# Kernel tuning notes

Measured on AMD Instinct MI355X. Metric: run time of the kernel, lower is better.

Reference implementation:

```python
import jax, jax.numpy as jnp
import numpy as np

TEMPERATURE = 0.5


def setup_inputs() -> dict:
    key = jax.random.key(0)
    k1, k2 = jax.random.split(key)
    N, D = 4096, 512
    emb_i = jax.random.normal(k1, (N, D), dtype=jnp.float32)
    emb_j = jax.random.normal(k2, (N, D), dtype=jnp.float32)
    return {"emb_i": emb_i, "emb_j": emb_j}


def reference(emb_i, emb_j):
    # L2-normalize each embedding row (F.normalize, dim=1)
    z_i = emb_i / jnp.linalg.norm(emb_i, axis=1, keepdims=True)
    z_j = emb_j / jnp.linalg.norm(emb_j, axis=1, keepdims=True)
    reps = jnp.concatenate([z_i, z_j], axis=0)  # [2N, D]
    N = emb_i.shape[0]
    M = 2 * N
    # cosine similarity of normalized vectors == dot product -> [2N, 2N]
    sim = jnp.einsum('id,jd->ij', reps, reps) / TEMPERATURE
    # denominator: sum_k!=i exp(sim[i,k]); original multiplies by one-hot complement
    exp_sim = jnp.exp(sim)
    denom = jnp.sum(exp_sim, axis=1) - jnp.diagonal(exp_sim)  # [2N]
    log_denom = jnp.log(denom)
    # positive pairs: (k, k+N) and (k+N, k)
    idx = jnp.arange(N)
    pos_ij = sim[idx, idx + N]          # sim(k, k+N)/T
    pos_ji = sim[idx + N, idx]          # sim(k+N, k)/T
    loss = jnp.sum(-(pos_ij - log_denom[:N]) - (pos_ji - log_denom[N:]))
    return loss / (2.0 * N)
```

## Files before the change

kernel.cpp:

```cpp
#include <hip/hip_runtime.h>
#include <cstdint>
#include <cstddef>

constexpr int N_ROWS = 4096;
constexpr int D      = 512;
constexpr int M      = 8192;
constexpr int NTILE  = 64;
constexpr int NBLK   = NTILE * (NTILE + 1) / 2;
constexpr int BKB    = 64;
constexpr int LDSB   = 128 * BKB;

using f32x4 = __attribute__((ext_vector_type(4))) float;
using ul2   = __attribute__((ext_vector_type(2))) unsigned long;

#define ASYNC_CP16(gsrc, ldst)                                                      \
    __builtin_amdgcn_global_load_lds(                                               \
        (const __attribute__((address_space(1))) unsigned int*)(gsrc),              \
        (__attribute__((address_space(3))) unsigned int*)(ldst), 16, 0, 0)

#define SS_FP8(pk, accum)                                                           \
    do {                                                                            \
        float f0 = __builtin_amdgcn_cvt_f32_fp8((pk), 0);                           \
        float f1 = __builtin_amdgcn_cvt_f32_fp8((pk), 1);                           \
        float f2 = __builtin_amdgcn_cvt_f32_fp8((pk), 2);                           \
        float f3 = __builtin_amdgcn_cvt_f32_fp8((pk), 3);                           \
        (accum) += f0 * f0 + f1 * f1 + f2 * f2 + f3 * f3;                           \
    } while (0)

__global__ __launch_bounds__(256) void normpos_kernel(
    const float* __restrict__ emb_i, const float* __restrict__ emb_j,
    uint8_t* __restrict__ zb, float* __restrict__ diagss,
    float* __restrict__ pos)
{
    const int wave = threadIdx.x >> 6, lane = threadIdx.x & 63;
    const int k = blockIdx.x * 4 + wave;

    const float4* a = (const float4*)(emb_i + (size_t)k * D);
    const float4* b = (const float4*)(emb_j + (size_t)k * D);
    float4 a0 = a[lane * 2], a1 = a[lane * 2 + 1];
    float4 b0 = b[lane * 2], b1 = b[lane * 2 + 1];

    float ssi = a0.x*a0.x + a0.y*a0.y + a0.z*a0.z + a0.w*a0.w
              + a1.x*a1.x + a1.y*a1.y + a1.z*a1.z + a1.w*a1.w;
    float ssj = b0.x*b0.x + b0.y*b0.y + b0.z*b0.z + b0.w*b0.w
              + b1.x*b1.x + b1.y*b1.y + b1.z*b1.z + b1.w*b1.w;
    float dp  = a0.x*b0.x + a0.y*b0.y + a0.z*b0.z + a0.w*b0.w
              + a1.x*b1.x + a1.y*b1.y + a1.z*b1.z + a1.w*b1.w;
    #pragma unroll
    for (int off = 32; off; off >>= 1) {
        ssi += __shfl_xor(ssi, off, 64);
        ssj += __shfl_xor(ssj, off, 64);
        dp  += __shfl_xor(dp,  off, 64);
    }
    const float invi = rsqrtf(ssi), invj = rsqrtf(ssj);

    const float zi[8] = {a0.x*invi, a0.y*invi, a0.z*invi, a0.w*invi,
                         a1.x*invi, a1.y*invi, a1.z*invi, a1.w*invi};
    const float zj[8] = {b0.x*invj, b0.y*invj, b0.z*invj, b0.w*invj,
                         b1.x*invj, b1.y*invj, b1.z*invj, b1.w*invj};

    int pi0 = __builtin_amdgcn_cvt_pk_fp8_f32(zi[0], zi[1], 0, false);
    pi0     = __builtin_amdgcn_cvt_pk_fp8_f32(zi[2], zi[3], pi0, true);
    int pi1 = __builtin_amdgcn_cvt_pk_fp8_f32(zi[4], zi[5], 0, false);
    pi1     = __builtin_amdgcn_cvt_pk_fp8_f32(zi[6], zi[7], pi1, true);
    int pj0 = __builtin_amdgcn_cvt_pk_fp8_f32(zj[0], zj[1], 0, false);
    pj0     = __builtin_amdgcn_cvt_pk_fp8_f32(zj[2], zj[3], pj0, true);
    int pj1 = __builtin_amdgcn_cvt_pk_fp8_f32(zj[4], zj[5], 0, false);
    pj1     = __builtin_amdgcn_cvt_pk_fp8_f32(zj[6], zj[7], pj1, true);

    float dssi = 0.f, dssj = 0.f;
    SS_FP8(pi0, dssi);
    SS_FP8(pi1, dssi);
    SS_FP8(pj0, dssj);
    SS_FP8(pj1, dssj);

    const int g = lane, bb = g >> 3, w = g & 7;
    const int sl = bb * 8 + ((w < 4) ? (w * 2) : ((w - 4) * 2 + 1));
    const unsigned long long vi =
        ((unsigned long long)(unsigned)pi1 << 32) | (unsigned)pi0;
    const unsigned long long vj =
        ((unsigned long long)(unsigned)pj1 << 32) | (unsigned)pj0;
    *(unsigned long long*)(zb + (size_t)k * D + sl * 8)            = vi;
    *(unsigned long long*)(zb + (size_t)(k + N_ROWS) * D + sl * 8) = vj;

    #pragma unroll
    for (int off = 32; off; off >>= 1) {
        dssi += __shfl_xor(dssi, off, 64);
        dssj += __shfl_xor(dssj, off, 64);
    }
    if (lane == 0) {
        diagss[k]          = dssi;
        diagss[k + N_ROWS] = dssj;
        pos[k]             = 2.0f * dp * invi * invj;
    }
}

__global__ __launch_bounds__(256, 4) void simgemm_kernel(
    const uint8_t* __restrict__ zb, float* __restrict__ partials)
{
    __shared__ ul2 AsV[2 * LDSB / 16];
    __shared__ ul2 BsV[2 * LDSB / 16];
    __shared__ float rp[4][64];
    __shared__ float cp4[4][64];
    uint8_t* As = (uint8_t*)AsV;
    uint8_t* Bs = (uint8_t*)BsV;

    const int tid  = threadIdx.x;
    const int wave = tid >> 6, lane = tid & 63;
    const int l15  = lane & 15, ks = lane >> 4;

    const int t = blockIdx.x;
    int bi = (int)((129.0f - sqrtf(129.0f * 129.0f - 8.0f * (float)t)) * 0.5f);
    while (bi > 0 && bi * (129 - bi) / 2 > t) --bi;
    while ((bi + 1) * (129 - (bi + 1)) / 2 <= t) ++bi;
    const int bj = bi + (t - bi * (129 - bi) / 2);
    const bool diag = (bi == bj);

    const int wrow = (wave >> 1) * 64, wcol = (wave & 1) * 64;

    const int srow = wave * 32 + (lane >> 2);
    const int scol = ((lane & 3) ^ ((lane >> 3) & 3)) * 16;
    const uint8_t* gA = zb + (size_t)(bi * 128 + srow) * D + scol;
    const uint8_t* gB = zb + (size_t)(bj * 128 + srow) * D + scol;
    uint8_t* lA = As + wave * 32 * BKB;
    uint8_t* lB = Bs + wave * 32 * BKB;

    ASYNC_CP16(gA,            lA);
    ASYNC_CP16(gA + 16 * D,   lA + 16 * BKB);
    ASYNC_CP16(gB,            lB);
    ASYNC_CP16(gB + 16 * D,   lB + 16 * BKB);

    f32x4 acc[4][4] = {};
    const int swb = (ks ^ ((l15 >> 1) & 3)) * 16;

    for (int it = 0; it < D / BKB; ++it) {
        __syncthreads();

        if (it + 1 < D / BKB) {
            const int kc  = (it + 1) * BKB;
            const int off = ((it + 1) & 1) * LDSB;
            ASYNC_CP16(gA + kc,          lA + off);
            ASYNC_CP16(gA + kc + 16 * D, lA + off + 16 * BKB);
            ASYNC_CP16(gB + kc,          lB + off);
            ASYNC_CP16(gB + kc + 16 * D, lB + off + 16 * BKB);
        }

        const int cb = (it & 1) * LDSB;
        ul2 af[4], bg[4];
        #pragma unroll
        for (int f = 0; f < 4; ++f) {
            af[f] = *(const ul2*)(As + cb + (wrow + f * 16 + l15) * BKB + swb);
            bg[f] = *(const ul2*)(Bs + cb + (wcol + f * 16 + l15) * BKB + swb);
        }
        #pragma unroll
        for (int i = 0; i < 4; ++i)
            #pragma unroll
            for (int j = 0; j < 4; ++j) {
                acc[i][j] = __builtin_amdgcn_mfma_f32_16x16x32_fp8_fp8(
                    (long)af[i][0], (long)bg[j][0], acc[i][j], 0, 0, 0);
                acc[i][j] = __builtin_amdgcn_mfma_f32_16x16x32_fp8_fp8(
                    (long)af[i][1], (long)bg[j][1], acc[i][j], 0, 0, 0);
            }
    }

    float rowp[4][4] = {};
    #pragma unroll
    for (int j = 0; j < 4; ++j) {
        float cpj = 0.f;
        #pragma unroll
        for (int i = 0; i < 4; ++i)
            #pragma unroll
            for (int r = 0; r < 4; ++r) {
                float e = __expf(2.0f * acc[i][j][r]);
                rowp[i][r] += e;
                cpj += e;
            }
        if (!diag) {
            cpj += __shfl_xor(cpj, 16, 64);
            cpj += __shfl_xor(cpj, 32, 64);
            if (ks == 0) cp4[wave][j * 16 + l15] = cpj;
        }
    }
    #pragma unroll
    for (int i = 0; i < 4; ++i)
        #pragma unroll
        for (int r = 0; r < 4; ++r) {
            float e = rowp[i][r];
            e += __shfl_xor(e, 1, 64);
            e += __shfl_xor(e, 2, 64);
            e += __shfl_xor(e, 4, 64);
            e += __shfl_xor(e, 8, 64);
            if (l15 == 0) rp[wave][i * 16 + ks * 4 + r] = e;
        }
    __syncthreads();

    float* pA = partials + (size_t)(bi * NTILE + bj) * 128;
    float* pB = partials + (size_t)(bj * NTILE + bi) * 128;
    if (tid < 128) {
        const int h = tid >> 6, rr = tid & 63;
        pA[tid] = rp[h * 2][rr] + rp[h * 2 + 1][rr];
    } else if (!diag) {
        const int c = tid - 128, h = c >> 6, cc = c & 63;
        pB[c] = cp4[h][cc] + cp4[h + 2][cc];
    }
}

__global__ __launch_bounds__(256) void rowfin_kernel(
    const float* __restrict__ partials, const float* __restrict__ diagss,
    const float* __restrict__ pos, float* __restrict__ lgpart)
{
    const int r  = blockIdx.x;
    const int ri = threadIdx.x & 127;
    const int ch = threadIdx.x >> 7;
    const float* base = partials + (size_t)r * NTILE * 128 + ri;
    float s = 0.f;
    #pragma unroll
    for (int c = 0; c < 32; ++c)
        s += base[(size_t)(ch * 32 + c) * 128];
    __shared__ float half1[128];
    __shared__ float red[4];
    if (ch == 1) half1[ri] = s;
    __syncthreads();
    float lg = 0.f;
    if (ch == 0) {
        float rs = s + half1[ri];
        int row = r * 128 + ri;
        lg = __logf(rs - __expf(2.0f * diagss[row]));
    }
    if (threadIdx.x < 64)
        lg -= 2.0f * pos[r * 64 + threadIdx.x];
    #pragma unroll
    for (int off = 32; off; off >>= 1) lg += __shfl_xor(lg, off, 64);
    const int wave = threadIdx.x >> 6, lane = threadIdx.x & 63;
    if (lane == 0) red[wave] = lg;
    __syncthreads();
    if (threadIdx.x == 0) lgpart[r] = red[0] + red[1] + red[2] + red[3];
}

__global__ __launch_bounds__(64) void loss_kernel(
    const float* __restrict__ lgpart, float* __restrict__ out)
{
    float local = lgpart[threadIdx.x];
    #pragma unroll
    for (int off = 32; off; off >>= 1) local += __shfl_xor(local, off, 64);
    if (threadIdx.x == 0) out[0] = local * (1.0f / 8192.0f);
}

extern "C" void kernel_launch(void* const* d_in, const int* in_sizes, int n_in,
                              void* d_out, int out_size, void* d_ws, size_t ws_size,
                              hipStream_t stream)
{
    const float* emb_i = (const float*)d_in[0];
    const float* emb_j = (const float*)d_in[1];

    uint8_t* zb = (uint8_t*)d_ws;
    float* partials = (float*)((char*)d_ws + (size_t)M * D);
    float* diagss   = partials + (size_t)NTILE * NTILE * 128;
    float* pos      = diagss + M;
    float* lgpart   = pos + N_ROWS;
    float* out      = (float*)d_out;

    normpos_kernel<<<N_ROWS / 4, 256, 0, stream>>>(emb_i, emb_j, zb, diagss, pos);
    simgemm_kernel<<<NBLK, 256, 0, stream>>>(zb, partials);
    rowfin_kernel<<<NTILE, 256, 0, stream>>>(partials, diagss, pos, lgpart);
    loss_kernel<<<1, 64, 0, stream>>>(lgpart, out);
}
```

Measured before the change: 103.4 us.

## Use 256x128 tiles with 512 threads and triple-buffered async LDS pipeline

Changes the symmetric similarity GEMM from 128x128 upper-triangular tiles with 256 threads to 256x128 jobs with 8 waves, where the A panel is shared by two row strips. It also replaces double buffering with a three-stage async global-to-LDS pipeline with explicit vmcnt/lgkmcnt waits, split MFMA phases and setprio hints. The aim is more operand reuse per load, fewer blocks and better overlap of memory with MFMA. The cost is a larger LDS footprint, which may lower occupancy, and a more intricate job indexing where diagonal jobs compute some redundant tiles.

```diff
diff --git a/kernel.cpp b/kernel.cpp
--- a/kernel.cpp
+++ b/kernel.cpp
@@ -6,9 +6,12 @@
 constexpr int D      = 512;
 constexpr int M      = 8192;
 constexpr int NTILE  = 64;
-constexpr int NBLK   = NTILE * (NTILE + 1) / 2;
+constexpr int NJOB   = 1056;
 constexpr int BKB    = 64;
-constexpr int LDSB   = 128 * BKB;
+constexpr int NKT    = D / BKB;
+constexpr int ATB    = 256 * BKB;
+constexpr int BTB    = 128 * BKB;
+constexpr int TILEB  = ATB + BTB;
 
 using f32x4 = __attribute__((ext_vector_type(4))) float;
 using ul2   = __attribute__((ext_vector_type(2))) unsigned long;
@@ -95,113 +98,146 @@
     }
 }
 
-__global__ __launch_bounds__(256, 4) void simgemm_kernel(
+#define MM2(AC, AF, BF)                                                             \
+    do {                                                                            \
+        AC = __builtin_amdgcn_mfma_f32_16x16x32_fp8_fp8(                            \
+                 (long)(AF)[0], (long)(BF)[0], AC, 0, 0, 0);                        \
+        AC = __builtin_amdgcn_mfma_f32_16x16x32_fp8_fp8(                            \
+                 (long)(AF)[1], (long)(BF)[1], AC, 0, 0, 0);                        \
+    } while (0)
+
+__global__ __launch_bounds__(512, 4) void simgemm_kernel(
     const uint8_t* __restrict__ zb, float* __restrict__ partials)
 {
-    __shared__ ul2 AsV[2 * LDSB / 16];
-    __shared__ ul2 BsV[2 * LDSB / 16];
-    __shared__ float rp[4][64];
-    __shared__ float cp4[4][64];
-    uint8_t* As = (uint8_t*)AsV;
-    uint8_t* Bs = (uint8_t*)BsV;
+    __shared__ ul2 ldsV[3 * TILEB / 16];
+    __shared__ float rp[8][64];
+    __shared__ float cp[8][64];
+    uint8_t* lds = (uint8_t*)ldsV;
 
     const int tid  = threadIdx.x;
     const int wave = tid >> 6, lane = tid & 63;
     const int l15  = lane & 15, ks = lane >> 4;
 
     const int t = blockIdx.x;
-    int bi = (int)((129.0f - sqrtf(129.0f * 129.0f - 8.0f * (float)t)) * 0.5f);
-    while (bi > 0 && bi * (129 - bi) / 2 > t) --bi;
-    while ((bi + 1) * (129 - (bi + 1)) / 2 <= t) ++bi;
-    const int bj = bi + (t - bi * (129 - bi) / 2);
-    const bool diag = (bi == bj);
-
-    const int wrow = (wave >> 1) * 64, wcol = (wave & 1) * 64;
-
-    const int srow = wave * 32 + (lane >> 2);
-    const int scol = ((lane & 3) ^ ((lane >> 3) & 3)) * 16;
-    const uint8_t* gA = zb + (size_t)(bi * 128 + srow) * D + scol;
-    const uint8_t* gB = zb + (size_t)(bj * 128 + srow) * D + scol;
-    uint8_t* lA = As + wave * 32 * BKB;
-    uint8_t* lB = Bs + wave * 32 * BKB;
-
-    ASYNC_CP16(gA,            lA);
-    ASYNC_CP16(gA + 16 * D,   lA + 16 * BKB);
-    ASYNC_CP16(gB,            lB);
-    ASYNC_CP16(gB + 16 * D,   lB + 16 * BKB);
+    int i = (int)((65.0f - sqrtf(4225.0f - 4.0f * (float)t)) * 0.5f);
+    if (i < 0) i = 0;
+    if (i > 31) i = 31;
+    while (i > 0 && i * (65 - i) > t) --i;
+    while ((i + 1) * (65 - (i + 1)) <= t) ++i;
+    const int j = 2 * i + (t - i * (65 - i));
+    const bool diagcls = (j - 2 * i) < 2;
+
+    const int srow = tid >> 2;
+    const int sch  = (tid & 3) ^ ((srow >> 1) & 3);
+    const uint8_t* gA = zb + (size_t)(i * 256 + srow) * D + sch * 16;
+    const uint8_t* gB = zb + (size_t)(j * 128 + srow) * D + sch * 16;
+    uint8_t* lw = lds + wave * 1024;
+
+#define STAGE(KT, BUF)                                                              \
+    do {                                                                            \
+        const uint8_t* _a = gA + (KT) * BKB;                                        \
+        const uint8_t* _b = gB + (KT) * BKB;                                        \
+        uint8_t* _l = lw + (BUF) * TILEB;                                           \
+        ASYNC_CP16(_a,           _l);                                               \
+        ASYNC_CP16(_a + 128 * D, _l + 8192);                                        \
+        ASYNC_CP16(_b,           _l + ATB);                                         \
+    } while (0)
+
+    const int wr  = wave >> 1, wc = wave & 1;
+    const int swb = (ks ^ ((l15 >> 1) & 3)) * 16;
+    const int aof = (wr * 64 + l15) * BKB + swb;
+    const int bof = ATB + (wc * 64 + l15) * BKB + swb;
 
     f32x4 acc[4][4] = {};
-    const int swb = (ks ^ ((l15 >> 1) & 3)) * 16;
-
-    for (int it = 0; it < D / BKB; ++it) {
-        __syncthreads();
-
-        if (it + 1 < D / BKB) {
-            const int kc  = (it + 1) * BKB;
-            const int off = ((it + 1) & 1) * LDSB;
-            ASYNC_CP16(gA + kc,          lA + off);
-            ASYNC_CP16(gA + kc + 16 * D, lA + off + 16 * BKB);
-            ASYNC_CP16(gB + kc,          lB + off);
-            ASYNC_CP16(gB + kc + 16 * D, lB + off + 16 * BKB);
+
+    STAGE(0, 0);
+    STAGE(1, 1);
+    asm volatile("s_waitcnt vmcnt(3)" ::: "memory");
+    __builtin_amdgcn_s_barrier();
+
+    #pragma unroll
+    for (int kt = 0; kt < NKT; ++kt) {
+        const uint8_t* La = lds + (kt % 3) * TILEB;
+
+        ul2 a0 = *(const ul2*)(La + aof);
+        ul2 a1 = *(const ul2*)(La + aof + 1024);
+        ul2 b0 = *(const ul2*)(La + bof);
+        ul2 b1 = *(const ul2*)(La + bof + 1024);
+        ul2 b2 = *(const ul2*)(La + bof + 2048);
+        ul2 b3 = *(const ul2*)(La + bof + 3072);
+        if (kt + 2 < NKT) STAGE(kt + 2, (kt + 2) % 3);
+        __builtin_amdgcn_s_barrier();
+        asm volatile("s_waitcnt lgkmcnt(0)" ::: "memory");
+        __builtin_amdgcn_sched_barrier(0);
+        __builtin_amdgcn_s_setprio(1);
+        MM2(acc[0][0], a0, b0); MM2(acc[0][1], a0, b1);
+        MM2(acc[0][2], a0, b2); MM2(acc[0][3], a0, b3);
+        MM2(acc[1][0], a1, b0); MM2(acc[1][1], a1, b1);
+        MM2(acc[1][2], a1, b2); MM2(acc[1][3], a1, b3);
+        __builtin_amdgcn_s_setprio(0);
+        __builtin_amdgcn_s_barrier();
+
+        ul2 a2 = *(const ul2*)(La + aof + 2048);
+        ul2 a3 = *(const ul2*)(La + aof + 3072);
+        __builtin_amdgcn_s_barrier();
+        asm volatile("s_waitcnt lgkmcnt(0)" ::: "memory");
+        __builtin_amdgcn_sched_barrier(0);
+        __builtin_amdgcn_s_setprio(1);
+        MM2(acc[2][0], a2, b0); MM2(acc[2][1], a2, b1);
+        MM2(acc[2][2], a2, b2); MM2(acc[2][3], a2, b3);
+        MM2(acc[3][0], a3, b0); MM2(acc[3][1], a3, b1);
+        MM2(acc[3][2], a3, b2); MM2(acc[3][3], a3, b3);
+        __builtin_amdgcn_s_setprio(0);
+        if (kt < NKT - 2) {
+            asm volatile("s_waitcnt vmcnt(3)" ::: "memory");
+        } else if (kt == NKT - 2) {
+            asm volatile("s_waitcnt vmcnt(0)" ::: "memory");
         }
-
-        const int cb = (it & 1) * LDSB;
-        ul2 af[4], bg[4];
-        #pragma unroll
-        for (int f = 0; f < 4; ++f) {
-            af[f] = *(const ul2*)(As + cb + (wrow + f * 16 + l15) * BKB + swb);
-            bg[f] = *(const ul2*)(Bs + cb + (wcol + f * 16 + l15) * BKB + swb);
-        }
-        #pragma unroll
-        for (int i = 0; i < 4; ++i)
-            #pragma unroll
-            for (int j = 0; j < 4; ++j) {
-                acc[i][j] = __builtin_amdgcn_mfma_f32_16x16x32_fp8_fp8(
-                    (long)af[i][0], (long)bg[j][0], acc[i][j], 0, 0, 0);
-                acc[i][j] = __builtin_amdgcn_mfma_f32_16x16x32_fp8_fp8(
-                    (long)af[i][1], (long)bg[j][1], acc[i][j], 0, 0, 0);
-            }
+        __builtin_amdgcn_s_barrier();
     }
 
     float rowp[4][4] = {};
     #pragma unroll
-    for (int j = 0; j < 4; ++j) {
+    for (int jj = 0; jj < 4; ++jj) {
         float cpj = 0.f;
         #pragma unroll
-        for (int i = 0; i < 4; ++i)
+        for (int ii = 0; ii < 4; ++ii)
             #pragma unroll
             for (int r = 0; r < 4; ++r) {
-                float e = __expf(2.0f * acc[i][j][r]);
-                rowp[i][r] += e;
+                float e = __expf(2.0f * acc[ii][jj][r]);
+                rowp[ii][r] += e;
                 cpj += e;
             }
-        if (!diag) {
+        if (!diagcls) {
             cpj += __shfl_xor(cpj, 16, 64);
             cpj += __shfl_xor(cpj, 32, 64);
-            if (ks == 0) cp4[wave][j * 16 + l15] = cpj;
+            if (ks == 0) cp[wave][jj * 16 + l15] = cpj;
         }
     }
     #pragma unroll
-    for (int i = 0; i < 4; ++i)
+    for (int ii = 0; ii < 4; ++ii)
         #pragma unroll
         for (int r = 0; r < 4; ++r) {
-            float e = rowp[i][r];
+            float e = rowp[ii][r];
             e += __shfl_xor(e, 1, 64);
             e += __shfl_xor(e, 2, 64);
             e += __shfl_xor(e, 4, 64);
             e += __shfl_xor(e, 8, 64);
-            if (l15 == 0) rp[wave][i * 16 + ks * 4 + r] = e;
+            if (l15 == 0) rp[wave][ii * 16 + ks * 4 + r] = e;
         }
     __syncthreads();
 
-    float* pA = partials + (size_t)(bi * NTILE + bj) * 128;
-    float* pB = partials + (size_t)(bj * NTILE + bi) * 128;
-    if (tid < 128) {
-        const int h = tid >> 6, rr = tid & 63;
-        pA[tid] = rp[h * 2][rr] + rp[h * 2 + 1][rr];
-    } else if (!diag) {
-        const int c = tid - 128, h = c >> 6, cc = c & 63;
-        pB[c] = cp4[h][cc] + cp4[h + 2][cc];
+    if (tid < 256) {
+        const int rl = tid & 63;
+        const float v = rp[(tid >> 6) * 2][rl] + rp[(tid >> 6) * 2 + 1][rl];
+        const int rc = 2 * i + (tid >> 7);
+        partials[((size_t)rc * NTILE + j) * 128 + (tid & 127)] = v;
+    } else if (!diagcls) {
+        const int c2 = tid - 256;
+        const int half = c2 >> 7, c = c2 & 127;
+        const int wcc = c >> 6, cl = c & 63;
+        const float v = cp[half * 4 + wcc][cl] + cp[half * 4 + 2 + wcc][cl];
+        partials[((size_t)j * NTILE + 2 * i + half) * 128 + c] = v;
     }
 }
 
@@ -261,7 +297,7 @@
     float* out      = (float*)d_out;
 
     normpos_kernel<<<N_ROWS / 4, 256, 0, stream>>>(emb_i, emb_j, zb, diagss, pos);
-    simgemm_kernel<<<NBLK, 256, 0, stream>>>(zb, partials);
+    simgemm_kernel<<<NJOB, 512, 0, stream>>>(zb, partials);
     rowfin_kernel<<<NTILE, 256, 0, stream>>>(partials, diagss, pos, lgpart);
     loss_kernel<<<1, 64, 0, stream>>>(lgpart, out);
 }
```

Measured after the change: 107.8 us. +4.3%, slower.

## Switch FP8 GEMM to 32x32x64 scaled MFMA with natural K layout

Applied to the files above, without the earlier changes.

Replaces the 16x16x32 FP8 MFMA tiling (4x4 fragments per wave) with the gfx950 32x32x64 f8f6f4 scaled MFMA (2x2 fragments), using unit scales. The normalization kernel now writes FP8 rows in natural order instead of the interleaved permutation, and each lane loads two 16-byte swizzled chunks to form the 32-byte operand. The epilogue row and column reductions are remapped to the 32x32 accumulator layout. The aim is fewer MFMA issues and LDS reads per K step. The trade-off is a larger accumulator per instruction and a more complex output index mapping that must be exactly right.

```diff
diff --git a/kernel.cpp b/kernel.cpp
--- a/kernel.cpp
+++ b/kernel.cpp
@@ -10,8 +10,10 @@
 constexpr int BKB    = 64;
 constexpr int LDSB   = 128 * BKB;
 
-using f32x4 = __attribute__((ext_vector_type(4))) float;
-using ul2   = __attribute__((ext_vector_type(2))) unsigned long;
+using f32x16 = __attribute__((ext_vector_type(16))) float;
+using i32x4  = __attribute__((ext_vector_type(4))) int;
+using i32x8  = __attribute__((ext_vector_type(8))) int;
+using ul2    = __attribute__((ext_vector_type(2))) unsigned long;
 
 #define ASYNC_CP16(gsrc, ldst)                                                      \
     __builtin_amdgcn_global_load_lds(                                               \
@@ -74,14 +76,12 @@
     SS_FP8(pj0, dssj);
     SS_FP8(pj1, dssj);
 
-    const int g = lane, bb = g >> 3, w = g & 7;
-    const int sl = bb * 8 + ((w < 4) ? (w * 2) : ((w - 4) * 2 + 1));
     const unsigned long long vi =
         ((unsigned long long)(unsigned)pi1 << 32) | (unsigned)pi0;
     const unsigned long long vj =
         ((unsigned long long)(unsigned)pj1 << 32) | (unsigned)pj0;
-    *(unsigned long long*)(zb + (size_t)k * D + sl * 8)            = vi;
-    *(unsigned long long*)(zb + (size_t)(k + N_ROWS) * D + sl * 8) = vj;
+    *(unsigned long long*)(zb + (size_t)k * D + lane * 8)            = vi;
+    *(unsigned long long*)(zb + (size_t)(k + N_ROWS) * D + lane * 8) = vj;
 
     #pragma unroll
     for (int off = 32; off; off >>= 1) {
@@ -107,7 +107,7 @@
 
     const int tid  = threadIdx.x;
     const int wave = tid >> 6, lane = tid & 63;
-    const int l15  = lane & 15, ks = lane >> 4;
+    const int l31  = lane & 31, half = lane >> 5;
 
     const int t = blockIdx.x;
     int bi = (int)((129.0f - sqrtf(129.0f * 129.0f - 8.0f * (float)t)) * 0.5f);
@@ -130,8 +130,8 @@
     ASYNC_CP16(gB,            lB);
     ASYNC_CP16(gB + 16 * D,   lB + 16 * BKB);
 
-    f32x4 acc[4][4] = {};
-    const int swb = (ks ^ ((l15 >> 1) & 3)) * 16;
+    f32x16 acc[2][2] = {};
+    const int c0b = ((2 * half) ^ ((l31 >> 1) & 3)) * 16;
 
     for (int it = 0; it < D / BKB; ++it) {
         __syncthreads();
@@ -146,51 +146,56 @@
         }
 
         const int cb = (it & 1) * LDSB;
-        ul2 af[4], bg[4];
-        #pragma unroll
-        for (int f = 0; f < 4; ++f) {
-            af[f] = *(const ul2*)(As + cb + (wrow + f * 16 + l15) * BKB + swb);
-            bg[f] = *(const ul2*)(Bs + cb + (wcol + f * 16 + l15) * BKB + swb);
-        }
-        #pragma unroll
-        for (int i = 0; i < 4; ++i)
+        i32x8 af[2], bf[2];
+        #pragma unroll
+        for (int f = 0; f < 2; ++f) {
+            const uint8_t* pa = As + cb + (size_t)(wrow + f * 32 + l31) * BKB;
+            i32x4 alo = *(const i32x4*)(pa + c0b);
+            i32x4 ahi = *(const i32x4*)(pa + (c0b ^ 16));
+            af[f] = __builtin_shufflevector(alo, ahi, 0, 1, 2, 3, 4, 5, 6, 7);
+            const uint8_t* pb = Bs + cb + (size_t)(wcol + f * 32 + l31) * BKB;
+            i32x4 blo = *(const i32x4*)(pb + c0b);
+            i32x4 bhi = *(const i32x4*)(pb + (c0b ^ 16));
+            bf[f] = __builtin_shufflevector(blo, bhi, 0, 1, 2, 3, 4, 5, 6, 7);
+        }
+        #pragma unroll
+        for (int i = 0; i < 2; ++i)
             #pragma unroll
-            for (int j = 0; j < 4; ++j) {
-                acc[i][j] = __builtin_amdgcn_mfma_f32_16x16x32_fp8_fp8(
-                    (long)af[i][0], (long)bg[j][0], acc[i][j], 0, 0, 0);
-                acc[i][j] = __builtin_amdgcn_mfma_f32_16x16x32_fp8_fp8(
-                    (long)af[i][1], (long)bg[j][1], acc[i][j], 0, 0, 0);
-            }
-    }
-
-    float rowp[4][4] = {};
-    #pragma unroll
-    for (int j = 0; j < 4; ++j) {
+            for (int j = 0; j < 2; ++j)
+                acc[i][j] = __builtin_amdgcn_mfma_scale_f32_32x32x64_f8f6f4(
+                    af[i], bf[j], acc[i][j], 0, 0,
+                    0, 0x7f7f7f7f, 0, 0x7f7f7f7f);
+    }
+
+    float rowp[2][16] = {};
+    #pragma unroll
+    for (int j = 0; j < 2; ++j) {
         float cpj = 0.f;
         #pragma unroll
-        for (int i = 0; i < 4; ++i)
+        for (int i = 0; i < 2; ++i)
             #pragma unroll
-            for (int r = 0; r < 4; ++r) {
+            for (int r = 0; r < 16; ++r) {
                 float e = __expf(2.0f * acc[i][j][r]);
                 rowp[i][r] += e;
                 cpj += e;
             }
         if (!diag) {
-            cpj += __shfl_xor(cpj, 16, 64);
             cpj += __shfl_xor(cpj, 32, 64);
-            if (ks == 0) cp4[wave][j * 16 + l15] = cpj;
-        }
-    }
-    #pragma unroll
-    for (int i = 0; i < 4; ++i)
-        #pragma unroll
-        for (int r = 0; r < 4; ++r) {
+            if (half == 0) cp4[wave][j * 32 + l31] = cpj;
+        }
+    }
+    #pragma unroll
+    for (int i = 0; i < 2; ++i)
+        #pragma unroll
+        for (int r = 0; r < 16; ++r) {
             float e = rowp[i][r];
             e += __shfl_xor(e, 1, 64);
             e += __shfl_xor(e, 2, 64);
             e += __shfl_xor(e, 4, 64);
             e += __shfl_xor(e, 8, 64);
-            if (l15 == 0) rp[wave][i * 16 + ks * 4 + r] = e;
+            e += __shfl_xor(e, 16, 64);
+            if (l31 == 0)
+                rp[wave][i * 32 + (r & 3) + 8 * (r >> 2) + 4 * half] = e;
         }
     __syncthreads();
 
```

Result: slower. 116.5 us (+12.7%).
